# Optimization experiments

Measured on AMD Instinct MI355X. Metric: run time of the kernel, lower is better.

The kernel has to match this reference:

```python
import jax, jax.numpy as jnp
import numpy as np

NUM_HEADS = 8
LN_EPS = 1e-5


def _ln(x, g, b):
    mu = x.mean(-1, keepdims=True)
    xc = x - mu
    v = (xc * xc).mean(-1, keepdims=True)
    return xc * jax.lax.rsqrt(v + LN_EPS) * g + b


def setup_inputs() -> dict:
    key = jax.random.key(0)
    B, T, D, NI, NT = 16, 512, 256, 85, 77
    L, FF, TH = 2, 1024, 32
    ks = iter(jax.random.split(key, 40))
    def nrm(shape, std):
        return jax.random.normal(next(ks), shape, jnp.float32) * std
    inp = {
        'img_tokens': nrm((B, NI, D), 1.0),
        'text_tokens': nrm((B, NT, D), 1.0),
        'task_tokens': nrm((T, D), 0.02),
        'type_task': nrm((D,), 0.02),
        'type_img': nrm((D,), 0.02),
        'type_txt': nrm((D,), 0.02),
        'in_ln_g': jnp.ones((D,), jnp.float32), 'in_ln_b': jnp.zeros((D,), jnp.float32),
        'Wqkv': nrm((L, 3 * D, D), 1.0 / np.sqrt(D)), 'bqkv': jnp.zeros((L, 3 * D), jnp.float32),
        'Wo': nrm((L, D, D), 1.0 / np.sqrt(D)), 'bo': jnp.zeros((L, D), jnp.float32),
        'ln1_g': jnp.ones((L, D), jnp.float32), 'ln1_b': jnp.zeros((L, D), jnp.float32),
        'ln2_g': jnp.ones((L, D), jnp.float32), 'ln2_b': jnp.zeros((L, D), jnp.float32),
        'W1': nrm((L, FF, D), 1.0 / np.sqrt(D)), 'b1': jnp.zeros((L, FF), jnp.float32),
        'W2': nrm((L, D, FF), 1.0 / np.sqrt(FF)), 'b2': jnp.zeros((L, D), jnp.float32),
        'out_ln_g': jnp.ones((D,), jnp.float32), 'out_ln_b': jnp.zeros((D,), jnp.float32),
        'tw1': nrm((T, TH, D), 1.0 / np.sqrt(D)), 'tb1': jnp.zeros((T, TH), jnp.float32),
        'tw2': nrm((T, TH), 1.0 / np.sqrt(TH)), 'tb2': jnp.zeros((T,), jnp.float32),
        'text_mask': jnp.arange(NT)[None, :] < jax.random.randint(next(ks), (B, 1), 10, NT + 1),
        'labels': jax.random.randint(next(ks), (B, T), -1, 2),
    }
    return inp


def reference(img_tokens, text_tokens, task_tokens, type_task, type_img, type_txt,
              in_ln_g, in_ln_b, Wqkv, bqkv, Wo, bo, ln1_g, ln1_b, ln2_g, ln2_b,
              W1, b1, W2, b2, out_ln_g, out_ln_b, tw1, tb1, tw2, tb2,
              text_mask, labels):
    B, NI, D = img_tokens.shape
    T = task_tokens.shape[0]
    L = Wqkv.shape[0]
    hd = D // NUM_HEADS
    available = labels != -1                                   # (B, T)
    n_avail = available.sum(axis=1)                            # (B,)
    # Route B: stable-sort available task ids to the front (permutation per row)
    order = jnp.argsort((~available).astype(jnp.int32), axis=1, stable=True)  # (B, T)
    task_toks = task_tokens[order] + type_task                 # (B, T, D)
    seq = jnp.concatenate([task_toks, img_tokens + type_img, text_tokens + type_txt], axis=1)
    seq = _ln(seq, in_ln_g, in_ln_b)
    task_pad = jnp.arange(T)[None, :] >= n_avail[:, None]
    pad = jnp.concatenate([task_pad, jnp.zeros((B, NI), bool), ~text_mask], axis=1)
    bias = jnp.where(pad, -1e9, 0.0).astype(seq.dtype)[:, None, None, :]  # key-padding mask
    scale = 1.0 / np.sqrt(hd)
    S = seq.shape[1]
    for l in range(L):  # pre-LN transformer encoder layers (eval mode)
        h = _ln(seq, ln1_g[l], ln1_b[l])
        qkv = h @ Wqkv[l].T + bqkv[l]
        q, k, v = jnp.split(qkv, 3, axis=-1)
        q = q.reshape(B, S, NUM_HEADS, hd)
        k = k.reshape(B, S, NUM_HEADS, hd)
        v = v.reshape(B, S, NUM_HEADS, hd)
        scores = jnp.einsum('bqhd,bkhd->bhqk', q, k) * scale + bias
        attn = jax.nn.softmax(scores, axis=-1)
        o = jnp.einsum('bhqk,bkhd->bqhd', attn, v).reshape(B, S, D)
        seq = seq + o @ Wo[l].T + bo[l]
        h2 = _ln(seq, ln2_g[l], ln2_b[l])
        seq = seq + jax.nn.gelu(h2 @ W1[l].T + b1[l], approximate=False) @ W2[l].T + b2[l]
    task_out = _ln(seq[:, :T], out_ln_g, out_ln_b)             # (B, T, D)
    # undo the per-row permutation so task t's token sits at column t, then
    # apply all per-task towers as one grouped matmul (MoE dispatch/combine)
    y = jnp.zeros_like(task_out).at[jnp.arange(B)[:, None], order].set(task_out)
    hsz = jax.nn.relu(jnp.einsum('btd,thd->bth', y, tw1) + tb1[None])
    out = jnp.einsum('bth,th->bt', hsz, tw2) + tb2[None]
    return jnp.where(available, out, jnp.zeros((), out.dtype))
```

## Files before the change

kernel.cpp:

```cpp
#include <hip/hip_runtime.h>
#include <hip/hip_bf16.h>
#include <math.h>

constexpr int B_  = 16;
constexpr int T_  = 512;
constexpr int D_  = 256;
constexpr int NI_ = 85;
constexpr int NT_ = 77;
constexpr int S_  = T_ + NI_ + NT_;
constexpr int M_  = B_ * S_;
constexpr int FF_ = 1024;
constexpr int TH_ = 32;
constexpr int NH_ = 8;
constexpr int KT_ = 704;
constexpr int NKT_ = KT_ / 64;

constexpr float MASK_NEG = -30000.0f;

constexpr int N_FT = 26;
constexpr int OFF_[N_FT + 1] = {
    0,
    348160,
    663552,
    794624,
    794880,
    795136,
    795392,
    795648,
    795904,
    1189120,
    1190656,
    1321728,
    1322240,
    1322752,
    1323264,
    1323776,
    1324288,
    1848576,
    1850624,
    2374912,
    2375424,
    2375680,
    2375936,
    6570240,
    6586624,
    6603008,
    6603520
};
constexpr int TOTAL_ELEMS = OFF_[N_FT];
constexpr int CONV_BLOCKS = (TOTAL_ELEMS + 511) / 512;

typedef __attribute__((ext_vector_type(8))) short bfrag;
typedef __attribute__((ext_vector_type(4))) float f32x4;

__device__ inline float bf2f(__hip_bfloat16 x) { return __bfloat162float(x); }
__device__ inline __hip_bfloat16 f2bf(float x) { return __float2bfloat16(x); }
__device__ inline float wsum64(float v) {
    #pragma unroll
    for (int m = 32; m >= 1; m >>= 1) v += __shfl_xor(v, m, 64);
    return v;
}
__device__ inline bool is_f32_mode(const void* ln_g_raw) {
    return (*(const unsigned int*)ln_g_raw) == 0x3F800000u;
}

__device__ inline bool tile_dead(int m0, int m1, const int* __restrict__ n_avail) {
    int b = m0 / S_;
    int base = b * S_;
    return (m0 >= base + n_avail[b]) && (m1 <= base + T_);
}

__device__ inline void gload_lds16(const __hip_bfloat16* g, __hip_bfloat16* l) {
#if defined(__has_builtin) && __has_builtin(__builtin_amdgcn_global_load_lds)
    __builtin_amdgcn_global_load_lds(
        (const __attribute__((address_space(1))) unsigned int*)g,
        (__attribute__((address_space(3))) unsigned int*)l, 16, 0, 0);
#else
    *reinterpret_cast<uint4*>(l) = *reinterpret_cast<const uint4*>(g);
#endif
}

struct Ptrs { const void* p[N_FT]; };

__global__ __launch_bounds__(512) void k_init(Ptrs ptrs, __hip_bfloat16* __restrict__ canon,
                                              const int* __restrict__ labels,
                                              int* __restrict__ inv,
                                              int* __restrict__ n_avail) {
    if (blockIdx.x < CONV_BLOCKS) {
        int idx = blockIdx.x * 512 + threadIdx.x;
        if (idx >= TOTAL_ELEMS) return;
        bool f32 = is_f32_mode(ptrs.p[6]);
        int t = 0;
        #pragma unroll
        for (int i = 1; i < N_FT; i++) if (idx >= OFF_[i]) t = i;
        int local = idx - OFF_[t];
        if (f32) canon[idx] = f2bf(((const float*)ptrs.p[t])[local]);
        else     canon[idx] = ((const __hip_bfloat16*)ptrs.p[t])[local];
    } else {
        __shared__ int sc[T_];
        int b = blockIdx.x - CONV_BLOCKS, t = threadIdx.x;
        int av = (labels[b * T_ + t] != -1) ? 1 : 0;
        sc[t] = av;
        __syncthreads();
        for (int off = 1; off < T_; off <<= 1) {
            int v = sc[t];
            int u = (t >= off) ? sc[t - off] : 0;
            __syncthreads();
            sc[t] = v + u;
            __syncthreads();
        }
        int incl  = sc[t];
        int excl  = incl - av;
        int total = sc[T_ - 1];
        inv[b * T_ + t] = av ? excl : (total + (t - excl));
        if (t == 0) n_avail[b] = total;
    }
}

__global__ void k_build(const __hip_bfloat16* __restrict__ img,
                        const __hip_bfloat16* __restrict__ txt,
                        const __hip_bfloat16* __restrict__ task,
                        const __hip_bfloat16* __restrict__ ty_task,
                        const __hip_bfloat16* __restrict__ ty_img,
                        const __hip_bfloat16* __restrict__ ty_txt,
                        const __hip_bfloat16* __restrict__ g,
                        const __hip_bfloat16* __restrict__ bln,
                        const __hip_bfloat16* __restrict__ g1,
                        const __hip_bfloat16* __restrict__ b1,
                        const void* __restrict__ text_mask,
                        const int* __restrict__ inv,
                        const int* __restrict__ n_avail,
                        float* __restrict__ seq,
                        __hip_bfloat16* __restrict__ h1,
                        float* __restrict__ bias) {
    int blk = blockIdx.x;
    int b = blk / S_, j = blk % S_;
    int lane = threadIdx.x;

    int dest;
    float bias_v;
    const __hip_bfloat16* src;
    const __hip_bfloat16* tvec;
    if (j < T_) {
        dest = inv[b * T_ + j];
        src = task + (size_t)j * D_;
        tvec = ty_task;
        bias_v = (dest >= n_avail[b]) ? MASK_NEG : 0.f;
    } else if (j < T_ + NI_) {
        dest = j;
        src = img + (size_t)(b * NI_ + (j - T_)) * D_;
        tvec = ty_img;
        bias_v = 0.f;
    } else {
        int x2 = j - T_ - NI_;
        dest = j;
        src = txt + (size_t)(b * NT_ + x2) * D_;
        tvec = ty_txt;
        const unsigned char* mb = (const unsigned char*)text_mask;
        bool is_byte = (mb[1] != 0);
        int mv = is_byte ? (int)mb[b * NT_ + x2]
                         : ((const int*)text_mask)[b * NT_ + x2];
        bias_v = mv ? 0.f : MASK_NEG;
    }

    float x[4];
    float s = 0.f, ss = 0.f;
    #pragma unroll
    for (int i = 0; i < 4; i++) {
        int d = lane * 4 + i;
        x[i] = bf2f(src[d]) + bf2f(tvec[d]);
        s += x[i];
        ss += x[i] * x[i];
    }
    s = wsum64(s);
    ss = wsum64(ss);
    float mean = s * (1.f / D_);
    float var  = ss * (1.f / D_) - mean * mean;
    float r    = rsqrtf(fmaxf(var, 0.f) + 1e-5f);

    float y[4];
    float s2 = 0.f, ss2 = 0.f;
    float* orow = seq + ((size_t)b * S_ + dest) * D_;
    #pragma unroll
    for (int i = 0; i < 4; i++) {
        int d = lane * 4 + i;
        y[i] = (x[i] - mean) * r * bf2f(g[d]) + bf2f(bln[d]);
        orow[d] = y[i];
        s2 += y[i];
        ss2 += y[i] * y[i];
    }
    s2 = wsum64(s2);
    ss2 = wsum64(ss2);
    float mean2 = s2 * (1.f / D_);
    float var2  = ss2 * (1.f / D_) - mean2 * mean2;
    float r2    = rsqrtf(fmaxf(var2, 0.f) + 1e-5f);
    __hip_bfloat16 tmp[4];
    #pragma unroll
    for (int i = 0; i < 4; i++) {
        int d = lane * 4 + i;
        tmp[i] = f2bf((y[i] - mean2) * r2 * bf2f(g1[d]) + bf2f(b1[d]));
    }
    *reinterpret_cast<uint2*>(h1 + ((size_t)b * S_ + dest) * D_ + lane * 4) =
        *reinterpret_cast<uint2*>(tmp);
    if (lane == 0) bias[b * S_ + dest] = bias_v;
}

template <int GELU>
__global__ __launch_bounds__(256) void k_gemm(const __hip_bfloat16* __restrict__ A,
                                              const __hip_bfloat16* __restrict__ W,
                                              const __hip_bfloat16* __restrict__ bias,
                                              __hip_bfloat16* __restrict__ Cout,
                                              const int* __restrict__ n_avail,
                                              int Mm, int N, int K) {
    constexpr int HALF = 12288;
    __shared__ __align__(16) __hip_bfloat16 Sh[2 * HALF];
    __hip_bfloat16* Es = Sh;

    int m0 = blockIdx.x * 64;
    if (tile_dead(m0, m0 + 64, n_avail)) return;
    int n0 = blockIdx.y * 128;
    int tid = threadIdx.x;
    int w = tid >> 6, lane = tid & 63;
    int lrow = lane & 15, quad = lane >> 4;
    int swz = lrow & 7;

    f32x4 acc[8] = {};

    int kq = (((tid & 7) ^ ((tid >> 3) & 7)) * 8);
    int arow = tid >> 3;
    const __hip_bfloat16* Ar0 = A + (size_t)min(m0 + arow,      Mm - 1) * K + kq;
    const __hip_bfloat16* Ar1 = A + (size_t)min(m0 + arow + 32, Mm - 1) * K + kq;
    const __hip_bfloat16* Wr[4];
    #pragma unroll
    for (int i = 0; i < 4; i++)
        Wr[i] = W + (size_t)(n0 + ((tid + i * 256) >> 3)) * K + kq;

    const int nsteps = K >> 6;

    {
        __hip_bfloat16* As0 = Sh;
        __hip_bfloat16* Ws0 = Sh + 4096;
        gload_lds16(Ar0, As0 + tid * 8);
        gload_lds16(Ar1, As0 + (tid + 256) * 8);
        #pragma unroll
        for (int i = 0; i < 4; i++) gload_lds16(Wr[i], Ws0 + (tid + i * 256) * 8);
    }
    __syncthreads();

    for (int ks = 0; ks < nsteps; ks++) {
        int curo = (ks & 1) * HALF;
        if (ks + 1 < nsteps) {
            int k1 = (ks + 1) << 6;
            __hip_bfloat16* Asn = Sh + (HALF - curo);
            __hip_bfloat16* Wsn = Asn + 4096;
            gload_lds16(Ar0 + k1, Asn + tid * 8);
            gload_lds16(Ar1 + k1, Asn + (tid + 256) * 8);
            #pragma unroll
            for (int i = 0; i < 4; i++) gload_lds16(Wr[i] + k1, Wsn + (tid + i * 256) * 8);
        }
        __hip_bfloat16* Asc = Sh + curo;
        __hip_bfloat16* Wsc = Asc + 4096;
        #pragma unroll
        for (int ko = 0; ko < 2; ko++) {
            int unit = ((ko * 4 + quad) ^ swz) << 3;
            bfrag af = *reinterpret_cast<const bfrag*>(&Asc[(w * 16 + lrow) * 64 + unit]);
            #pragma unroll
            for (int nt = 0; nt < 8; nt++) {
                bfrag bf = *reinterpret_cast<const bfrag*>(&Wsc[(nt * 16 + lrow) * 64 + unit]);
                acc[nt] = __builtin_amdgcn_mfma_f32_16x16x32_bf16(af, bf, acc[nt], 0, 0, 0);
            }
        }
        __syncthreads();
    }

    #pragma unroll
    for (int nt = 0; nt < 8; nt++) {
        int col = nt * 16 + lrow;
        float bv = bf2f(bias[n0 + col]);
        #pragma unroll
        for (int rg = 0; rg < 4; rg++) {
            int row = w * 16 + quad * 4 + rg;
            float v = acc[nt][rg] + bv;
            if (GELU) v = 0.5f * v * (1.f + erff(v * 0.70710678118654752f));
            Es[row * 136 + col] = f2bf(v);
        }
    }
    __syncthreads();

    #pragma unroll
    for (int i = 0; i < 4; i++) {
        int c = tid + i * 256;
        int row = c >> 4, off = (c & 15) * 8;
        int gm = m0 + row;
        if (gm < Mm) {
            uint4 v4 = *reinterpret_cast<const uint4*>(&Es[row * 136 + off]);
            *reinterpret_cast<uint4*>(&Cout[(size_t)gm * N + n0 + off]) = v4;
        }
    }
}

template <int LNOUT>
__global__ __launch_bounds__(256) void k_gemm_lnres(const __hip_bfloat16* __restrict__ A,
                                                    const __hip_bfloat16* __restrict__ W,
                                                    const __hip_bfloat16* __restrict__ bias,
                                                    float* __restrict__ seq,
                                                    const __hip_bfloat16* __restrict__ lng,
                                                    const __hip_bfloat16* __restrict__ lnb,
                                                    __hip_bfloat16* __restrict__ lnout,
                                                    const int* __restrict__ n_avail,
                                                    int K) {
    constexpr int N = 256;
    constexpr int ESTRIDE = 260;
    constexpr int HALF = 18432;
    __shared__ __align__(16) __hip_bfloat16 Sh[2 * HALF];
    float* Es = (float*)Sh;

    int m0 = blockIdx.x * 32;
    if (tile_dead(m0, m0 + 32, n_avail)) return;
    int tid = threadIdx.x;
    int w = tid >> 6, lane = tid & 63;
    int lrow = lane & 15, quad = lane >> 4;
    int swz = lrow & 7;

    f32x4 acc[2][4] = {};

    int kq = (((tid & 7) ^ ((tid >> 3) & 7)) * 8);
    const __hip_bfloat16* Ar = A + (size_t)(m0 + (tid >> 3)) * K + kq;
    const __hip_bfloat16* Wr[8];
    #pragma unroll
    for (int i = 0; i < 8; i++)
        Wr[i] = W + (size_t)((tid + i * 256) >> 3) * K + kq;

    const int nsteps = K >> 6;

    {
        __hip_bfloat16* As0 = Sh;
        __hip_bfloat16* Ws0 = Sh + 2048;
        gload_lds16(Ar, As0 + tid * 8);
        #pragma unroll
        for (int i = 0; i < 8; i++) gload_lds16(Wr[i], Ws0 + (tid + i * 256) * 8);
    }
    __syncthreads();

    for (int ks = 0; ks < nsteps; ks++) {
        int curo = (ks & 1) * HALF;
        if (ks + 1 < nsteps) {
            int k1 = (ks + 1) << 6;
            __hip_bfloat16* Asn = Sh + (HALF - curo);
            __hip_bfloat16* Wsn = Asn + 2048;
            gload_lds16(Ar + k1, Asn + tid * 8);
            #pragma unroll
            for (int i = 0; i < 8; i++) gload_lds16(Wr[i] + k1, Wsn + (tid + i * 256) * 8);
        }
        __hip_bfloat16* Asc = Sh + curo;
        __hip_bfloat16* Wsc = Asc + 2048;
        #pragma unroll
        for (int ko = 0; ko < 2; ko++) {
            int unit = ((ko * 4 + quad) ^ swz) << 3;
            bfrag af[2], bf[4];
            #pragma unroll
            for (int mt = 0; mt < 2; mt++)
                af[mt] = *reinterpret_cast<const bfrag*>(&Asc[(mt * 16 + lrow) * 64 + unit]);
            #pragma unroll
            for (int nt = 0; nt < 4; nt++)
                bf[nt] = *reinterpret_cast<const bfrag*>(&Wsc[(w * 64 + nt * 16 + lrow) * 64 + unit]);
            #pragma unroll
            for (int mt = 0; mt < 2; mt++)
                #pragma unroll
                for (int nt = 0; nt < 4; nt++)
                    acc[mt][nt] = __builtin_amdgcn_mfma_f32_16x16x32_bf16(af[mt], bf[nt], acc[mt][nt], 0, 0, 0);
        }
        __syncthreads();
    }

    #pragma unroll
    for (int nt = 0; nt < 4; nt++) {
        int col = w * 64 + nt * 16 + lrow;
        float bv = bf2f(bias[col]);
        #pragma unroll
        for (int mt = 0; mt < 2; mt++)
            #pragma unroll
            for (int rg = 0; rg < 4; rg++)
                Es[(mt * 16 + quad * 4 + rg) * ESTRIDE + col] = acc[mt][nt][rg] + bv;
    }
    __syncthreads();

    int row = tid >> 3, part = tid & 7;
    size_t gm = (size_t)(m0 + row);
    float* seqrow = seq + gm * N + part * 32;
    float t[32];
    float s = 0.f, ss = 0.f;
    #pragma unroll
    for (int j = 0; j < 8; j++) {
        float4 e = *reinterpret_cast<const float4*>(&Es[row * ESTRIDE + part * 32 + j * 4]);
        float4 r4 = *reinterpret_cast<const float4*>(&seqrow[j * 4]);
        float v0 = e.x + r4.x, v1 = e.y + r4.y, v2 = e.z + r4.z, v3 = e.w + r4.w;
        t[j * 4 + 0] = v0; t[j * 4 + 1] = v1; t[j * 4 + 2] = v2; t[j * 4 + 3] = v3;
        s += v0 + v1 + v2 + v3;
        ss += v0 * v0 + v1 * v1 + v2 * v2 + v3 * v3;
    }
    #pragma unroll
    for (int j = 0; j < 8; j++) {
        float4 o = make_float4(t[j * 4 + 0], t[j * 4 + 1], t[j * 4 + 2], t[j * 4 + 3]);
        *reinterpret_cast<float4*>(&seqrow[j * 4]) = o;
    }
    if (LNOUT) {
        #pragma unroll
        for (int mm = 4; mm >= 1; mm >>= 1) {
            s  += __shfl_xor(s,  mm, 8);
            ss += __shfl_xor(ss, mm, 8);
        }
        float mean = s * (1.f / N);
        float var  = ss * (1.f / N) - mean * mean;
        float r    = rsqrtf(fmaxf(var, 0.f) + 1e-5f);
        __hip_bfloat16 ob[32];
        #pragma unroll
        for (int j = 0; j < 32; j++) {
            int col = part * 32 + j;
            ob[j] = f2bf((t[j] - mean) * r * bf2f(lng[col]) + bf2f(lnb[col]));
        }
        #pragma unroll
        for (int j = 0; j < 4; j++)
            *reinterpret_cast<uint4*>(&lnout[gm * N + part * 32 + j * 8]) =
                *reinterpret_cast<const uint4*>(&ob[j * 8]);
    }
}

__global__ __launch_bounds__(256) void k_fattn(const __hip_bfloat16* __restrict__ qkv,
                                               const float* __restrict__ bias,
                                               const int* __restrict__ n_avail,
                                               __hip_bfloat16* __restrict__ out) {
    __shared__ __align__(16) __hip_bfloat16 Vt[2][32 * 72];
    __shared__ __align__(16) __hip_bfloat16 Ps[4][32 * 72];
    __shared__ float Bs[KT_];
    __shared__ int alive[NKT_];
    __shared__ int tlist[NKT_ + 1];
    __shared__ int nact_s;
    int b = blockIdx.z, h = blockIdx.y;
    int q0b = blockIdx.x * 128;
    if (q0b >= n_avail[b] && q0b + 128 <= T_) return;
    int tid = threadIdx.x;
    int wave = tid >> 6, lane = tid & 63;
    int lrow = lane & 15, quad = lane >> 4;
    int q0 = q0b + wave * 32;

    const float scale = 0.17677669529663687f;
    const __hip_bfloat16* base = qkv + (size_t)b * S_ * 768;
    const float* brow = bias + b * S_;

    if (tid < NKT_) alive[tid] = 0;
    __syncthreads();
    for (int i = tid; i < KT_; i += 256) {
        float v = (i < S_) ? brow[i] : MASK_NEG;
        Bs[i] = v;
        if (v != MASK_NEG) alive[i >> 6] = 1;
    }
    __syncthreads();
    if (tid == 0) {
        int n = 0;
        for (int t = 0; t < NKT_; t++) if (alive[t]) tlist[n++] = t;
        if (n == 0) { tlist[0] = 0; n = 1; }
        tlist[n] = tlist[n - 1];
        nact_s = n;
    }
    __syncthreads();
    int nact = nact_s;

    bfrag qf[2];
    {
        int qr0 = min(q0 + lrow, S_ - 1);
        int qr1 = min(q0 + 16 + lrow, S_ - 1);
        qf[0] = *reinterpret_cast<const bfrag*>(base + (size_t)qr0 * 768 + h * 32 + quad * 8);
        qf[1] = *reinterpret_cast<const bfrag*>(base + (size_t)qr1 * 768 + h * 32 + quad * 8);
    }

    bfrag ones_f;
    #pragma unroll
    for (int i = 0; i < 8; i++) ((short*)&ones_f)[i] = (short)0x3F80;

    float m[2][4];
    #pragma unroll
    for (int qh = 0; qh < 2; qh++)
        #pragma unroll
        for (int rg = 0; rg < 4; rg++) m[qh][rg] = -3e38f;
    f32x4 Lacc[2] = {};
    f32x4 O[2][2] = {};

    int skey = lane;
    int sd   = wave * 8;

    bfrag kf_cur[4], vv_cur;
    {
        int k0 = tlist[0] * 64;
        #pragma unroll
        for (int nt = 0; nt < 4; nt++) {
            int kr = min(k0 + nt * 16 + lrow, S_ - 1);
            kf_cur[nt] = *reinterpret_cast<const bfrag*>(base + (size_t)kr * 768 + 256 + h * 32 + quad * 8);
        }
        int kr = min(k0 + skey, S_ - 1);
        vv_cur = *reinterpret_cast<const bfrag*>(base + (size_t)kr * 768 + 512 + h * 32 + sd);
    }

    for (int i = 0; i < nact; i++) {
        int k0 = tlist[i] * 64;
        __hip_bfloat16* vb = Vt[i & 1];

        #pragma unroll
        for (int j = 0; j < 8; j++) vb[(sd + j) * 72 + skey] = ((const __hip_bfloat16*)&vv_cur)[j];
        __syncthreads();

        bfrag kf_nxt[4], vv_nxt;
        {
            int kb = tlist[i + 1] * 64;
            #pragma unroll
            for (int nt = 0; nt < 4; nt++) {
                int kr = min(kb + nt * 16 + lrow, S_ - 1);
                kf_nxt[nt] = *reinterpret_cast<const bfrag*>(base + (size_t)kr * 768 + 256 + h * 32 + quad * 8);
            }
            int kr = min(kb + skey, S_ - 1);
            vv_nxt = *reinterpret_cast<const bfrag*>(base + (size_t)kr * 768 + 512 + h * 32 + sd);
        }

        f32x4 sc[2][4];
        #pragma unroll
        for (int nt = 0; nt < 4; nt++) {
            float bv = Bs[k0 + nt * 16 + lrow];
            #pragma unroll
            for (int qh = 0; qh < 2; qh++) {
                f32x4 z = {};
                sc[qh][nt] = __builtin_amdgcn_mfma_f32_16x16x32_bf16(qf[qh], kf_cur[nt], z, 0, 0, 0);
                #pragma unroll
                for (int rg = 0; rg < 4; rg++) sc[qh][nt][rg] = sc[qh][nt][rg] * scale + bv;
            }
        }

        #pragma unroll
        for (int qh = 0; qh < 2; qh++) {
            float alpha[4];
            #pragma unroll
            for (int rg = 0; rg < 4; rg++) {
                float rm = fmaxf(fmaxf(sc[qh][0][rg], sc[qh][1][rg]), fmaxf(sc[qh][2][rg], sc[qh][3][rg]));
                #pragma unroll
                for (int mm2 = 1; mm2 <= 8; mm2 <<= 1) rm = fmaxf(rm, __shfl_xor(rm, mm2, 64));
                float mn = fmaxf(m[qh][rg], rm);
                alpha[rg] = __expf(m[qh][rg] - mn);
                m[qh][rg] = mn;
                #pragma unroll
                for (int nt = 0; nt < 4; nt++) sc[qh][nt][rg] = __expf(sc[qh][nt][rg] - mn);
            }
            #pragma unroll
            for (int rg = 0; rg < 4; rg++) {
                O[qh][0][rg] *= alpha[rg];
                O[qh][1][rg] *= alpha[rg];
                Lacc[qh][rg] *= alpha[rg];
            }
            #pragma unroll
            for (int nt = 0; nt < 4; nt++)
                #pragma unroll
                for (int rg = 0; rg < 4; rg++)
                    Ps[wave][(qh * 16 + quad * 4 + rg) * 72 + nt * 16 + lrow] = f2bf(sc[qh][nt][rg]);
        }

        #pragma unroll
        for (int qh = 0; qh < 2; qh++) {
            bfrag ap0 = *reinterpret_cast<const bfrag*>(&Ps[wave][(qh * 16 + lrow) * 72 + quad * 8]);
            bfrag ap1 = *reinterpret_cast<const bfrag*>(&Ps[wave][(qh * 16 + lrow) * 72 + 32 + quad * 8]);
            #pragma unroll
            for (int dt = 0; dt < 2; dt++) {
                bfrag bv0 = *reinterpret_cast<const bfrag*>(&vb[(dt * 16 + lrow) * 72 + quad * 8]);
                bfrag bv1 = *reinterpret_cast<const bfrag*>(&vb[(dt * 16 + lrow) * 72 + 32 + quad * 8]);
                O[qh][dt] = __builtin_amdgcn_mfma_f32_16x16x32_bf16(ap0, bv0, O[qh][dt], 0, 0, 0);
                O[qh][dt] = __builtin_amdgcn_mfma_f32_16x16x32_bf16(ap1, bv1, O[qh][dt], 0, 0, 0);
            }
            Lacc[qh] = __builtin_amdgcn_mfma_f32_16x16x32_bf16(ap0, ones_f, Lacc[qh], 0, 0, 0);
            Lacc[qh] = __builtin_amdgcn_mfma_f32_16x16x32_bf16(ap1, ones_f, Lacc[qh], 0, 0, 0);
        }

        #pragma unroll
        for (int nt = 0; nt < 4; nt++) kf_cur[nt] = kf_nxt[nt];
        vv_cur = vv_nxt;
    }

    #pragma unroll
    for (int qh = 0; qh < 2; qh++)
        #pragma unroll
        for (int rg = 0; rg < 4; rg++) {
            int qrow = q0 + qh * 16 + quad * 4 + rg;
            if (qrow < S_) {
                float invl = 1.f / Lacc[qh][rg];
                #pragma unroll
                for (int dt = 0; dt < 2; dt++)
                    out[((size_t)b * S_ + qrow) * D_ + h * 32 + dt * 16 + lrow] = f2bf(O[qh][dt][rg] * invl);
            }
        }
}

__global__ __launch_bounds__(256) void k_final(const float* __restrict__ seq,
                                               const int* __restrict__ inv,
                                               const int* __restrict__ labels,
                                               const __hip_bfloat16* __restrict__ g,
                                               const __hip_bfloat16* __restrict__ bb,
                                               const __hip_bfloat16* __restrict__ tw1,
                                               const __hip_bfloat16* __restrict__ tb1,
                                               const __hip_bfloat16* __restrict__ tw2,
                                               const __hip_bfloat16* __restrict__ tb2,
                                               const void* __restrict__ ln_g_raw,
                                               void* __restrict__ out) {
    int idx = blockIdx.x;
    int t = idx >> 4, b = idx & 15;
    int tid = threadIdx.x;
    bool f32o = is_f32_mode(ln_g_raw);

    int lab = labels[b * T_ + t];
    if (lab == -1) {
        if (tid == 0) {
            if (f32o) ((float*)out)[b * T_ + t] = 0.f;
            else      ((__hip_bfloat16*)out)[b * T_ + t] = f2bf(0.f);
        }
        return;
    }

    __shared__ float y[D_];
    __shared__ float hb[TH_];
    __shared__ float rs[4], rq[4];

    int row = inv[b * T_ + t];
    float x = seq[((size_t)b * S_ + row) * D_ + tid];
    float s1 = wsum64(x);
    float s2 = wsum64(x * x);
    int w = tid >> 6, lane = tid & 63;
    if (lane == 0) { rs[w] = s1; rq[w] = s2; }
    __syncthreads();
    float fs = rs[0] + rs[1] + rs[2] + rs[3];
    float fq = rq[0] + rq[1] + rq[2] + rq[3];
    float mean = fs * (1.f / D_);
    float var  = fq * (1.f / D_) - mean * mean;
    float r    = rsqrtf(fmaxf(var, 0.f) + 1e-5f);
    y[tid] = (x - mean) * r * bf2f(g[tid]) + bf2f(bb[tid]);
    __syncthreads();

    int hh = tid >> 3, part = tid & 7;
    const uint4* w4 = reinterpret_cast<const uint4*>(tw1 + ((size_t)t * TH_ + hh) * D_ + part * 32);
    float acc = 0.f;
    #pragma unroll
    for (int i = 0; i < 4; i++) {
        uint4 kv = w4[i];
        unsigned int wd[4] = {kv.x, kv.y, kv.z, kv.w};
        #pragma unroll
        for (int j2 = 0; j2 < 4; j2++) {
            unsigned int lo = wd[j2] << 16, hi = wd[j2] & 0xffff0000u;
            float flo, fhi;
            __builtin_memcpy(&flo, &lo, 4);
            __builtin_memcpy(&fhi, &hi, 4);
            acc += y[part * 32 + i * 8 + j2 * 2] * flo;
            acc += y[part * 32 + i * 8 + j2 * 2 + 1] * fhi;
        }
    }
    #pragma unroll
    for (int mm = 4; mm >= 1; mm >>= 1) acc += __shfl_down(acc, mm, 8);
    if (part == 0) {
        float hz = acc + bf2f(tb1[t * TH_ + hh]);
        hz = fmaxf(hz, 0.f);
        hb[hh] = hz * bf2f(tw2[t * TH_ + hh]);
    }
    __syncthreads();
    if (tid == 0) {
        float o = bf2f(tb2[t]);
        #pragma unroll
        for (int i = 0; i < TH_; i++) o += hb[i];
        if (f32o) ((float*)out)[b * T_ + t] = o;
        else      ((__hip_bfloat16*)out)[b * T_ + t] = f2bf(o);
    }
}

extern "C" void kernel_launch(void* const* d_in, const int* in_sizes, int n_in,
                              void* d_out, int out_size, void* d_ws, size_t ws_size,
                              hipStream_t stream) {
    const void* tmask  = d_in[26];
    const int*  labels = (const int*)d_in[27];

    char* p = (char*)d_ws;
    auto alloc = [&](size_t bytes) {
        char* r = p;
        p += (bytes + 255) & ~size_t(255);
        return r;
    };
    __hip_bfloat16* canon  = (__hip_bfloat16*)alloc(sizeof(__hip_bfloat16) * (size_t)TOTAL_ELEMS);
    int*            inv     = (int*)alloc(sizeof(int) * B_ * T_);
    int*            n_avail = (int*)alloc(sizeof(int) * B_);
    float*          bias    = (float*)alloc(sizeof(float) * M_);
    float*          seqF    = (float*)alloc(sizeof(float) * (size_t)M_ * D_);
    __hip_bfloat16* bufA    = (__hip_bfloat16*)alloc(sizeof(__hip_bfloat16) * (size_t)M_ * D_);
    __hip_bfloat16* bufBig  = (__hip_bfloat16*)alloc(sizeof(__hip_bfloat16) * (size_t)M_ * FF_);

    Ptrs ptrs;
    for (int i = 0; i < N_FT; i++) ptrs.p[i] = d_in[i];
    hipLaunchKernelGGL(k_init, dim3(CONV_BLOCKS + B_), dim3(512), 0, stream,
                       ptrs, canon, labels, inv, n_avail);

    const __hip_bfloat16* img      = canon + OFF_[0];
    const __hip_bfloat16* txt      = canon + OFF_[1];
    const __hip_bfloat16* task     = canon + OFF_[2];
    const __hip_bfloat16* ty_task  = canon + OFF_[3];
    const __hip_bfloat16* ty_img   = canon + OFF_[4];
    const __hip_bfloat16* ty_txt   = canon + OFF_[5];
    const __hip_bfloat16* in_ln_g  = canon + OFF_[6];
    const __hip_bfloat16* in_ln_b  = canon + OFF_[7];
    const __hip_bfloat16* Wqkv     = canon + OFF_[8];
    const __hip_bfloat16* bqkv     = canon + OFF_[9];
    const __hip_bfloat16* Wo       = canon + OFF_[10];
    const __hip_bfloat16* bo       = canon + OFF_[11];
    const __hip_bfloat16* ln1_g    = canon + OFF_[12];
    const __hip_bfloat16* ln1_b    = canon + OFF_[13];
    const __hip_bfloat16* ln2_g    = canon + OFF_[14];
    const __hip_bfloat16* ln2_b    = canon + OFF_[15];
    const __hip_bfloat16* W1       = canon + OFF_[16];
    const __hip_bfloat16* b1       = canon + OFF_[17];
    const __hip_bfloat16* W2       = canon + OFF_[18];
    const __hip_bfloat16* b2       = canon + OFF_[19];
    const __hip_bfloat16* out_ln_g = canon + OFF_[20];
    const __hip_bfloat16* out_ln_b = canon + OFF_[21];
    const __hip_bfloat16* tw1      = canon + OFF_[22];
    const __hip_bfloat16* tb1      = canon + OFF_[23];
    const __hip_bfloat16* tw2      = canon + OFF_[24];
    const __hip_bfloat16* tb2      = canon + OFF_[25];

    hipLaunchKernelGGL(k_build, dim3(B_ * S_), dim3(64), 0, stream,
                       img, txt, task, ty_task, ty_img, ty_txt, in_ln_g, in_ln_b,
                       ln1_g, ln1_b, tmask, inv, n_avail, seqF, bufA, bias);

    const int mtiles = (M_ + 63) / 64;
    const int rtiles = M_ / 32;
    const int qtiles = (S_ + 127) / 128;

    for (int l = 0; l < 2; l++) {
        hipLaunchKernelGGL((k_gemm<0>), dim3(mtiles, 6), dim3(256), 0, stream,
                           bufA, Wqkv + (size_t)l * 3 * D_ * D_, bqkv + l * 3 * D_,
                           bufBig, n_avail, M_, 3 * D_, D_);
        hipLaunchKernelGGL(k_fattn, dim3(qtiles, NH_, B_), dim3(256), 0, stream,
                           bufBig, bias, n_avail, bufA);
        hipLaunchKernelGGL((k_gemm_lnres<1>), dim3(rtiles), dim3(256), 0, stream,
                           bufA, Wo + (size_t)l * D_ * D_, bo + l * D_, seqF,
                           ln2_g + l * D_, ln2_b + l * D_, bufA, n_avail, D_);
        hipLaunchKernelGGL((k_gemm<1>), dim3(mtiles, 8), dim3(256), 0, stream,
                           bufA, W1 + (size_t)l * FF_ * D_, b1 + l * FF_,
                           bufBig, n_avail, M_, FF_, D_);
        if (l == 0) {
            hipLaunchKernelGGL((k_gemm_lnres<1>), dim3(rtiles), dim3(256), 0, stream,
                               bufBig, W2 + (size_t)l * D_ * FF_, b2 + l * D_, seqF,
                               ln1_g + 1 * D_, ln1_b + 1 * D_, bufA, n_avail, FF_);
        } else {
            hipLaunchKernelGGL((k_gemm_lnres<0>), dim3(rtiles), dim3(256), 0, stream,
                               bufBig, W2 + (size_t)l * D_ * FF_, b2 + l * D_, seqF,
                               (const __hip_bfloat16*)nullptr, (const __hip_bfloat16*)nullptr,
                               (__hip_bfloat16*)nullptr, n_avail, FF_);
        }
    }

    hipLaunchKernelGGL(k_final, dim3(T_ * B_), dim3(256), 0, stream,
                       seqF, inv, labels, out_ln_g, out_ln_b,
                       tw1, tb1, tw2, tb2, d_in[6], d_out);
}
```

Measured before the change: 381.3 us.

## Fuse Wo projection, LN2, FFN up/GELU/down and residual into one kernel

Replaces three launches per layer (Wo GEMM with residual+LN, W1 GEMM with GELU, W2 GEMM with residual+LN) with a single kernel per 32-row tile. The LN2 output and the GELU intermediate stay in LDS in 128-wide FF chunks, so the large FF activation buffer is never written to or read from global memory. In exchange each block streams all of W1 and W2 from L2, the loads are no longer double-buffered, and only a few hundred blocks each carry much longer serial work, which lowers occupancy and parallelism.

```diff
diff --git a/kernel.cpp b/kernel.cpp
--- a/kernel.cpp
+++ b/kernel.cpp
@@ -80,6 +80,10 @@
 #endif
 }
 
+__device__ inline float gelu_f(float v) {
+    return 0.5f * v * (1.f + erff(v * 0.70710678118654752f));
+}
+
 struct Ptrs { const void* p[N_FT]; };
 
 __global__ __launch_bounds__(512) void k_init(Ptrs ptrs, __hip_bfloat16* __restrict__ canon,
@@ -281,7 +285,7 @@
         for (int rg = 0; rg < 4; rg++) {
             int row = w * 16 + quad * 4 + rg;
             float v = acc[nt][rg] + bv;
-            if (GELU) v = 0.5f * v * (1.f + erff(v * 0.70710678118654752f));
+            if (GELU) v = gelu_f(v);
             Es[row * 136 + col] = f2bf(v);
         }
     }
@@ -300,20 +304,25 @@
 }
 
 template <int LNOUT>
-__global__ __launch_bounds__(256) void k_gemm_lnres(const __hip_bfloat16* __restrict__ A,
-                                                    const __hip_bfloat16* __restrict__ W,
-                                                    const __hip_bfloat16* __restrict__ bias,
-                                                    float* __restrict__ seq,
-                                                    const __hip_bfloat16* __restrict__ lng,
-                                                    const __hip_bfloat16* __restrict__ lnb,
-                                                    __hip_bfloat16* __restrict__ lnout,
-                                                    const int* __restrict__ n_avail,
-                                                    int K) {
-    constexpr int N = 256;
+__global__ __launch_bounds__(256) void k_ffnmega(const __hip_bfloat16* __restrict__ A,
+                                                 const __hip_bfloat16* __restrict__ Wop,
+                                                 const __hip_bfloat16* __restrict__ bop,
+                                                 const __hip_bfloat16* __restrict__ ln2g,
+                                                 const __hip_bfloat16* __restrict__ ln2b,
+                                                 const __hip_bfloat16* __restrict__ W1p,
+                                                 const __hip_bfloat16* __restrict__ b1p,
+                                                 const __hip_bfloat16* __restrict__ W2p,
+                                                 const __hip_bfloat16* __restrict__ b2p,
+                                                 float* __restrict__ seq,
+                                                 const __hip_bfloat16* __restrict__ g1n,
+                                                 const __hip_bfloat16* __restrict__ b1n,
+                                                 __hip_bfloat16* __restrict__ lnout,
+                                                 const int* __restrict__ n_avail) {
+    constexpr int PT_OFF  = 0;
+    constexpr int WST_OFF = 4096;
+    constexpr int HT_OFF  = 20480;
     constexpr int ESTRIDE = 260;
-    constexpr int HALF = 18432;
-    __shared__ __align__(16) __hip_bfloat16 Sh[2 * HALF];
-    float* Es = (float*)Sh;
+    __shared__ __align__(16) __hip_bfloat16 Sh[28672];
 
     int m0 = blockIdx.x * 32;
     if (tile_dead(m0, m0 + 32, n_avail)) return;
@@ -321,62 +330,47 @@
     int w = tid >> 6, lane = tid & 63;
     int lrow = lane & 15, quad = lane >> 4;
     int swz = lrow & 7;
+    int kq = ((tid & 7) ^ ((tid >> 3) & 7)) * 8;
 
     f32x4 acc[2][4] = {};
-
-    int kq = (((tid & 7) ^ ((tid >> 3) & 7)) * 8);
-    const __hip_bfloat16* Ar = A + (size_t)(m0 + (tid >> 3)) * K + kq;
-    const __hip_bfloat16* Wr[8];
-    #pragma unroll
-    for (int i = 0; i < 8; i++)
-        Wr[i] = W + (size_t)((tid + i * 256) >> 3) * K + kq;
-
-    const int nsteps = K >> 6;
-
     {
-        __hip_bfloat16* As0 = Sh;
-        __hip_bfloat16* Ws0 = Sh + 2048;
-        gload_lds16(Ar, As0 + tid * 8);
-        #pragma unroll
-        for (int i = 0; i < 8; i++) gload_lds16(Wr[i], Ws0 + (tid + i * 256) * 8);
-    }
-    __syncthreads();
-
-    for (int ks = 0; ks < nsteps; ks++) {
-        int curo = (ks & 1) * HALF;
-        if (ks + 1 < nsteps) {
-            int k1 = (ks + 1) << 6;
-            __hip_bfloat16* Asn = Sh + (HALF - curo);
-            __hip_bfloat16* Wsn = Asn + 2048;
-            gload_lds16(Ar + k1, Asn + tid * 8);
-            #pragma unroll
-            for (int i = 0; i < 8; i++) gload_lds16(Wr[i] + k1, Wsn + (tid + i * 256) * 8);
-        }
-        __hip_bfloat16* Asc = Sh + curo;
-        __hip_bfloat16* Wsc = Asc + 2048;
-        #pragma unroll
-        for (int ko = 0; ko < 2; ko++) {
-            int unit = ((ko * 4 + quad) ^ swz) << 3;
-            bfrag af[2], bf[4];
-            #pragma unroll
-            for (int mt = 0; mt < 2; mt++)
-                af[mt] = *reinterpret_cast<const bfrag*>(&Asc[(mt * 16 + lrow) * 64 + unit]);
-            #pragma unroll
-            for (int nt = 0; nt < 4; nt++)
-                bf[nt] = *reinterpret_cast<const bfrag*>(&Wsc[(w * 64 + nt * 16 + lrow) * 64 + unit]);
-            #pragma unroll
-            for (int mt = 0; mt < 2; mt++)
+        const __hip_bfloat16* Ar = A + (size_t)(m0 + (tid >> 3)) * 256 + kq;
+        __hip_bfloat16* As = Sh;
+        __hip_bfloat16* Ws = Sh + 2048;
+        for (int ks = 0; ks < 4; ks++) {
+            int k0 = ks << 6;
+            if (ks) __syncthreads();
+            gload_lds16(Ar + k0, As + tid * 8);
+            #pragma unroll
+            for (int i = 0; i < 8; i++)
+                gload_lds16(Wop + (size_t)((tid + i * 256) >> 3) * 256 + k0 + kq,
+                            Ws + (tid + i * 256) * 8);
+            __syncthreads();
+            #pragma unroll
+            for (int ko = 0; ko < 2; ko++) {
+                int unit = ((ko * 4 + quad) ^ swz) << 3;
+                bfrag af[2], bf[4];
+                #pragma unroll
+                for (int mt = 0; mt < 2; mt++)
+                    af[mt] = *reinterpret_cast<const bfrag*>(&As[(mt * 16 + lrow) * 64 + unit]);
                 #pragma unroll
                 for (int nt = 0; nt < 4; nt++)
-                    acc[mt][nt] = __builtin_amdgcn_mfma_f32_16x16x32_bf16(af[mt], bf[nt], acc[mt][nt], 0, 0, 0);
+                    bf[nt] = *reinterpret_cast<const bfrag*>(&Ws[(w * 64 + nt * 16 + lrow) * 64 + unit]);
+                #pragma unroll
+                for (int mt = 0; mt < 2; mt++)
+                    #pragma unroll
+                    for (int nt = 0; nt < 4; nt++)
+                        acc[mt][nt] = __builtin_amdgcn_mfma_f32_16x16x32_bf16(af[mt], bf[nt], acc[mt][nt], 0, 0, 0);
+            }
         }
         __syncthreads();
     }
 
+    float* Es = (float*)Sh;
     #pragma unroll
     for (int nt = 0; nt < 4; nt++) {
         int col = w * 64 + nt * 16 + lrow;
-        float bv = bf2f(bias[col]);
+        float bv = bf2f(bop[col]);
         #pragma unroll
         for (int mt = 0; mt < 2; mt++)
             #pragma unroll
@@ -387,12 +381,12 @@
 
     int row = tid >> 3, part = tid & 7;
     size_t gm = (size_t)(m0 + row);
-    float* seqrow = seq + gm * N + part * 32;
+    const float* seqrow = seq + gm * 256 + part * 32;
     float t[32];
     float s = 0.f, ss = 0.f;
     #pragma unroll
     for (int j = 0; j < 8; j++) {
-        float4 e = *reinterpret_cast<const float4*>(&Es[row * ESTRIDE + part * 32 + j * 4]);
+        float4 e  = *reinterpret_cast<const float4*>(&Es[row * ESTRIDE + part * 32 + j * 4]);
         float4 r4 = *reinterpret_cast<const float4*>(&seqrow[j * 4]);
         float v0 = e.x + r4.x, v1 = e.y + r4.y, v2 = e.z + r4.z, v3 = e.w + r4.w;
         t[j * 4 + 0] = v0; t[j * 4 + 1] = v1; t[j * 4 + 2] = v2; t[j * 4 + 3] = v3;
@@ -400,28 +394,154 @@
         ss += v0 * v0 + v1 * v1 + v2 * v2 + v3 * v3;
     }
     #pragma unroll
+    for (int mm = 4; mm >= 1; mm >>= 1) {
+        s  += __shfl_xor(s,  mm, 8);
+        ss += __shfl_xor(ss, mm, 8);
+    }
+    {
+        float mean = s * (1.f / 256);
+        float var  = ss * (1.f / 256) - mean * mean;
+        float r    = rsqrtf(fmaxf(var, 0.f) + 1e-5f);
+        __hip_bfloat16* Ht = Sh + HT_OFF;
+        #pragma unroll
+        for (int jj = 0; jj < 4; jj++) {
+            __hip_bfloat16 hb[8];
+            #pragma unroll
+            for (int k = 0; k < 8; k++) {
+                int col = part * 32 + jj * 8 + k;
+                hb[k] = f2bf((t[jj * 8 + k] - mean) * r * bf2f(ln2g[col]) + bf2f(ln2b[col]));
+            }
+            int unit = (part * 4 + jj) ^ (row & 7);
+            *reinterpret_cast<uint4*>(&Ht[row * 256 + unit * 8]) =
+                *reinterpret_cast<const uint4*>(hb);
+        }
+    }
+    __syncthreads();
+
+    f32x4 acc2[2][4] = {};
+    __hip_bfloat16* Wst = Sh + WST_OFF;
+    __hip_bfloat16* Pt  = Sh + PT_OFF;
+    __hip_bfloat16* Ht  = Sh + HT_OFF;
+
+    for (int c = 0; c < 8; c++) {
+        int ff0 = c << 7;
+        f32x4 pacc[2][2] = {};
+        for (int ks = 0; ks < 4; ks++) {
+            if (c | ks) __syncthreads();
+            #pragma unroll
+            for (int i = 0; i < 4; i++) {
+                int u = tid + i * 256;
+                gload_lds16(W1p + (size_t)(ff0 + (u >> 3)) * 256 + (ks << 6) + kq,
+                            Wst + u * 8);
+            }
+            __syncthreads();
+            #pragma unroll
+            for (int ko = 0; ko < 2; ko++) {
+                int hunit = ((ks * 8 + ko * 4 + quad) ^ swz) << 3;
+                int wunit = ((ko * 4 + quad) ^ swz) << 3;
+                bfrag af[2], bf[2];
+                #pragma unroll
+                for (int mt = 0; mt < 2; mt++)
+                    af[mt] = *reinterpret_cast<const bfrag*>(&Ht[(mt * 16 + lrow) * 256 + hunit]);
+                #pragma unroll
+                for (int nt = 0; nt < 2; nt++)
+                    bf[nt] = *reinterpret_cast<const bfrag*>(&Wst[(w * 32 + nt * 16 + lrow) * 64 + wunit]);
+                #pragma unroll
+                for (int mt = 0; mt < 2; mt++)
+                    #pragma unroll
+                    for (int nt = 0; nt < 2; nt++)
+                        pacc[mt][nt] = __builtin_amdgcn_mfma_f32_16x16x32_bf16(af[mt], bf[nt], pacc[mt][nt], 0, 0, 0);
+            }
+        }
+        __syncthreads();
+
+        #pragma unroll
+        for (int mt = 0; mt < 2; mt++)
+            #pragma unroll
+            for (int nt = 0; nt < 2; nt++)
+                #pragma unroll
+                for (int rg = 0; rg < 4; rg++) {
+                    int prow = mt * 16 + quad * 4 + rg;
+                    int pcol = w * 32 + nt * 16 + lrow;
+                    float v = pacc[mt][nt][rg] + bf2f(b1p[ff0 + pcol]);
+                    v = gelu_f(v);
+                    int unit = (pcol >> 3) ^ (prow & 7);
+                    Pt[prow * 128 + unit * 8 + (pcol & 7)] = f2bf(v);
+                }
+
+        for (int ks2 = 0; ks2 < 2; ks2++) {
+            if (ks2) __syncthreads();
+            #pragma unroll
+            for (int i = 0; i < 8; i++) {
+                int u = tid + i * 256;
+                gload_lds16(W2p + (size_t)(u >> 3) * 1024 + ff0 + (ks2 << 6) + kq,
+                            Wst + u * 8);
+            }
+            __syncthreads();
+            #pragma unroll
+            for (int ko = 0; ko < 2; ko++) {
+                int punit = ((ks2 * 8 + ko * 4 + quad) ^ swz) << 3;
+                int wunit = ((ko * 4 + quad) ^ swz) << 3;
+                bfrag af2[2], bf2v[4];
+                #pragma unroll
+                for (int mt = 0; mt < 2; mt++)
+                    af2[mt] = *reinterpret_cast<const bfrag*>(&Pt[(mt * 16 + lrow) * 128 + punit]);
+                #pragma unroll
+                for (int nt = 0; nt < 4; nt++)
+                    bf2v[nt] = *reinterpret_cast<const bfrag*>(&Wst[(w * 64 + nt * 16 + lrow) * 64 + wunit]);
+                #pragma unroll
+                for (int mt = 0; mt < 2; mt++)
+                    #pragma unroll
+                    for (int nt = 0; nt < 4; nt++)
+                        acc2[mt][nt] = __builtin_amdgcn_mfma_f32_16x16x32_bf16(af2[mt], bf2v[nt], acc2[mt][nt], 0, 0, 0);
+            }
+        }
+    }
+    __syncthreads();
+
+    float* Es2 = (float*)Sh;
+    #pragma unroll
+    for (int nt = 0; nt < 4; nt++) {
+        int col = w * 64 + nt * 16 + lrow;
+        float bv = bf2f(b2p[col]);
+        #pragma unroll
+        for (int mt = 0; mt < 2; mt++)
+            #pragma unroll
+            for (int rg = 0; rg < 4; rg++)
+                Es2[(mt * 16 + quad * 4 + rg) * ESTRIDE + col] = acc2[mt][nt][rg] + bv;
+    }
+    __syncthreads();
+
+    float* seqw = seq + gm * 256 + part * 32;
+    float s2 = 0.f, ss2 = 0.f;
+    #pragma unroll
     for (int j = 0; j < 8; j++) {
-        float4 o = make_float4(t[j * 4 + 0], t[j * 4 + 1], t[j * 4 + 2], t[j * 4 + 3]);
-        *reinterpret_cast<float4*>(&seqrow[j * 4]) = o;
+        float4 e = *reinterpret_cast<const float4*>(&Es2[row * ESTRIDE + part * 32 + j * 4]);
+        float v0 = t[j * 4 + 0] + e.x, v1 = t[j * 4 + 1] + e.y;
+        float v2 = t[j * 4 + 2] + e.z, v3 = t[j * 4 + 3] + e.w;
+        t[j * 4 + 0] = v0; t[j * 4 + 1] = v1; t[j * 4 + 2] = v2; t[j * 4 + 3] = v3;
+        s2 += v0 + v1 + v2 + v3;
+        ss2 += v0 * v0 + v1 * v1 + v2 * v2 + v3 * v3;
+        *reinterpret_cast<float4*>(&seqw[j * 4]) = make_float4(v0, v1, v2, v3);
     }
     if (LNOUT) {
         #pragma unroll
         for (int mm = 4; mm >= 1; mm >>= 1) {
-            s  += __shfl_xor(s,  mm, 8);
-            ss += __shfl_xor(ss, mm, 8);
-        }
-        float mean = s * (1.f / N);
-        float var  = ss * (1.f / N) - mean * mean;
+            s2  += __shfl_xor(s2,  mm, 8);
+            ss2 += __shfl_xor(ss2, mm, 8);
+        }
+        float mean = s2 * (1.f / 256);
+        float var  = ss2 * (1.f / 256) - mean * mean;
         float r    = rsqrtf(fmaxf(var, 0.f) + 1e-5f);
         __hip_bfloat16 ob[32];
         #pragma unroll
         for (int j = 0; j < 32; j++) {
             int col = part * 32 + j;
-            ob[j] = f2bf((t[j] - mean) * r * bf2f(lng[col]) + bf2f(lnb[col]));
+            ob[j] = f2bf((t[j] - mean) * r * bf2f(g1n[col]) + bf2f(b1n[col]));
         }
         #pragma unroll
         for (int j = 0; j < 4; j++)
-            *reinterpret_cast<uint4*>(&lnout[gm * N + part * 32 + j * 8]) =
+            *reinterpret_cast<uint4*>(&lnout[gm * 256 + part * 32 + j * 8]) =
                 *reinterpret_cast<const uint4*>(&ob[j * 8]);
     }
 }
@@ -739,21 +859,24 @@
                            bufBig, n_avail, M_, 3 * D_, D_);
         hipLaunchKernelGGL(k_fattn, dim3(qtiles, NH_, B_), dim3(256), 0, stream,
                            bufBig, bias, n_avail, bufA);
-        hipLaunchKernelGGL((k_gemm_lnres<1>), dim3(rtiles), dim3(256), 0, stream,
-                           bufA, Wo + (size_t)l * D_ * D_, bo + l * D_, seqF,
-                           ln2_g + l * D_, ln2_b + l * D_, bufA, n_avail, D_);
-        hipLaunchKernelGGL((k_gemm<1>), dim3(mtiles, 8), dim3(256), 0, stream,
-                           bufA, W1 + (size_t)l * FF_ * D_, b1 + l * FF_,
-                           bufBig, n_avail, M_, FF_, D_);
         if (l == 0) {
-            hipLaunchKernelGGL((k_gemm_lnres<1>), dim3(rtiles), dim3(256), 0, stream,
-                               bufBig, W2 + (size_t)l * D_ * FF_, b2 + l * D_, seqF,
-                               ln1_g + 1 * D_, ln1_b + 1 * D_, bufA, n_avail, FF_);
+            hipLaunchKernelGGL((k_ffnmega<1>), dim3(rtiles), dim3(256), 0, stream,
+                               bufA,
+                               Wo + (size_t)l * D_ * D_, bo + l * D_,
+                               ln2_g + l * D_, ln2_b + l * D_,
+                               W1 + (size_t)l * FF_ * D_, b1 + l * FF_,
+                               W2 + (size_t)l * D_ * FF_, b2 + l * D_,
+                               seqF, ln1_g + 1 * D_, ln1_b + 1 * D_, bufA, n_avail);
         } else {
-            hipLaunchKernelGGL((k_gemm_lnres<0>), dim3(rtiles), dim3(256), 0, stream,
-                               bufBig, W2 + (size_t)l * D_ * FF_, b2 + l * D_, seqF,
-                               (const __hip_bfloat16*)nullptr, (const __hip_bfloat16*)nullptr,
-                               (__hip_bfloat16*)nullptr, n_avail, FF_);
+            hipLaunchKernelGGL((k_ffnmega<0>), dim3(rtiles), dim3(256), 0, stream,
+                               bufA,
+                               Wo + (size_t)l * D_ * D_, bo + l * D_,
+                               ln2_g + l * D_, ln2_b + l * D_,
+                               W1 + (size_t)l * FF_ * D_, b1 + l * FF_,
+                               W2 + (size_t)l * D_ * FF_, b2 + l * D_,
+                               seqF, (const __hip_bfloat16*)nullptr,
+                               (const __hip_bfloat16*)nullptr,
+                               (__hip_bfloat16*)nullptr, n_avail);
         }
     }
 
```

After: 366.1 us. 1.04x faster.
